# Performance work log

Hardware: AMD Instinct MI355X
Metric: run time of the kernel (lower is better)

## Reference

```python
import jax, jax.numpy as jnp
import numpy as np

N_NODES = 50000
N_EDGES = 800000
IN_DIM = 256
OUT_DIM = 64
HEADS = 4
NEG_SLOPE = 0.2  # PyG GATConv default


def setup_inputs() -> dict:
    key = jax.random.key(0)
    k_x, k_e, k_w, k_as, k_ad = jax.random.split(key, 5)
    x = jax.random.normal(k_x, (N_NODES, IN_DIM), dtype=jnp.float32)
    edge_index = jax.random.randint(k_e, (2, N_EDGES), 0, N_NODES, dtype=jnp.int64)
    # Glorot-ish scaled params (as in PyG GATConv)
    W = jax.random.normal(k_w, (IN_DIM, HEADS * OUT_DIM), dtype=jnp.float32) / np.sqrt(IN_DIM)
    att_src = jax.random.normal(k_as, (HEADS, OUT_DIM), dtype=jnp.float32) / np.sqrt(OUT_DIM)
    att_dst = jax.random.normal(k_ad, (HEADS, OUT_DIM), dtype=jnp.float32) / np.sqrt(OUT_DIM)
    bias = jnp.zeros((HEADS * OUT_DIM,), dtype=jnp.float32)
    return {"x": x, "edge_index": edge_index, "W": W,
            "att_src": att_src, "att_dst": att_dst, "bias": bias}


def reference(x, edge_index, W, att_src, att_dst, bias):
    N = x.shape[0]
    H, C = att_src.shape
    # add self-loops (PyG GATConv default add_self_loops=True)
    loop = jnp.arange(N, dtype=edge_index.dtype)
    src = jnp.concatenate([edge_index[0], loop])  # [E+N] message sources j
    dst = jnp.concatenate([edge_index[1], loop])  # [E+N] message targets i

    xh = (x @ W).reshape(N, H, C)                 # [N, H, C]
    a_src = jnp.einsum('nhc,hc->nh', xh, att_src)  # [N, H]
    a_dst = jnp.einsum('nhc,hc->nh', xh, att_dst)  # [N, H]

    logits = jax.nn.leaky_relu(a_src[src] + a_dst[dst], NEG_SLOPE)  # [E+N, H]
    # segment softmax over incoming edges of each destination node
    seg_max = jax.ops.segment_max(logits, dst, num_segments=N)      # [N, H]
    e = jnp.exp(logits - seg_max[dst])
    seg_sum = jax.ops.segment_sum(e, dst, num_segments=N)           # [N, H]
    alpha = e / seg_sum[dst]                                        # [E+N, H]

    # weighted scatter-aggregate of source features
    msgs = alpha[:, :, None] * xh[src]                              # [E+N, H, C]
    out = jax.ops.segment_sum(msgs, dst, num_segments=N)            # [N, H, C]
    out = out.reshape(N, H * C) + bias                              # concat heads + bias
    # h.dim() == 2 here, so the original's mean(dim=1) branch is not taken
    return out
```

## Files before the change

kernel.cpp:

```cpp
#include <hip/hip_runtime.h>

#define NEG_SLOPE 0.2f
#define LRELU(x) ((x) > 0.0f ? (x) : NEG_SLOPE * (x))

typedef short short8 __attribute__((ext_vector_type(8)));
typedef unsigned short ushort8 __attribute__((ext_vector_type(8)));
typedef float f32x4v __attribute__((ext_vector_type(4)));

__device__ __forceinline__ unsigned short f2bf(float f) {
  unsigned int u = __float_as_uint(f);
  unsigned int r = (u + 0x7FFFu + ((u >> 16) & 1u)) >> 16;
  return (unsigned short)r;
}

__device__ __forceinline__ float bf2f(unsigned short u) {
  return __uint_as_float(((unsigned int)u) << 16);
}

__device__ __forceinline__ unsigned int cvt_pk_bf16(float lo, float hi) {
  unsigned int r;
  asm("v_cvt_pk_bf16_f32 %0, %1, %2" : "=v"(r) : "v"(lo), "v"(hi));
  return r;
}

__device__ __forceinline__ void gload_lds16(const void* g, void* l) {
  __builtin_amdgcn_global_load_lds(
      (const __attribute__((address_space(1))) unsigned int*)g,
      (__attribute__((address_space(3))) unsigned int*)l, 16, 0, 0);
}

#define CBC 448
#define CBW 64
#define CBF 1024

__global__ __launch_bounds__(256) void fused_pre(
    const float* __restrict__ W, unsigned short* __restrict__ Wtb,
    const int* __restrict__ ei, int* __restrict__ deg,
    int* __restrict__ rank, int E) {
  int b = blockIdx.x;
  int tid = threadIdx.x;
  if (b < CBC) {
    for (int e = b * 256 + tid; e < E; e += CBC * 256)
      rank[e] = atomicAdd(&deg[ei[E + e]], 1);
  } else {
    int bb = b - CBC;
    for (int idx = bb * 256 + tid; idx < 256 * 256; idx += CBW * 256) {
      int n = idx >> 8, k = idx & 255;
      Wtb[n * 256 + k] = f2bf(W[k * 256 + n]);
    }
  }
}

__global__ __launch_bounds__(1024) void scan1_kernel(const int* __restrict__ deg,
                                                     int* __restrict__ row_start,
                                                     int* __restrict__ bsum, int N) {
  __shared__ int buf[1024];
  int i = blockIdx.x * 1024 + (int)threadIdx.x;
  int v = (i < N) ? deg[i] : 0;
  buf[threadIdx.x] = v;
  __syncthreads();
  int run = v;
  for (int off = 1; off < 1024; off <<= 1) {
    int t = ((int)threadIdx.x >= off) ? buf[threadIdx.x - off] : 0;
    __syncthreads();
    run += t;
    buf[threadIdx.x] = run;
    __syncthreads();
  }
  if (i < N) row_start[i] = run - v;
  if (threadIdx.x == 1023) bsum[blockIdx.x] = run;
}

__global__ __launch_bounds__(1024) void scan_off(int* __restrict__ row_start,
                                                 const int* __restrict__ bsum,
                                                 int nb, int N) {
  __shared__ int s_off;
  int b = blockIdx.x;
  if (threadIdx.x < 64) {
    int acc = 0;
    for (int j = (int)threadIdx.x; j < b; j += 64) acc += bsum[j];
    for (int off = 32; off; off >>= 1) acc += __shfl_down(acc, off, 64);
    if (threadIdx.x == 0) s_off = acc;
  }
  __syncthreads();
  int off = s_off;
  int i = b * 1024 + (int)threadIdx.x;
  if (i < N) row_start[i] += off;
  if (b == nb - 1 && threadIdx.x == 0) row_start[N] = off + bsum[b];
}

__global__ __launch_bounds__(256) void fill_kernel(
    const int* __restrict__ ei, const int* __restrict__ row_start,
    const int* __restrict__ rank, int* __restrict__ csr_src, int E) {
  for (int e = blockIdx.x * 256 + threadIdx.x; e < E; e += CBF * 256)
    csr_src[row_start[ei[E + e]] + rank[e]] = ei[e];
}

__global__ __launch_bounds__(256) void gemm_mfma(
    const float* __restrict__ Xf, const unsigned short* __restrict__ Wtb,
    const float* __restrict__ attS, const float* __restrict__ attD,
    unsigned short* __restrict__ XHb, float* __restrict__ a_src,
    float* __restrict__ a_dst, int N) {
  __shared__ unsigned short lA[128 * 32];
  __shared__ unsigned short lB[128 * 32];
  const int gb = blockIdx.x;
  const int tid = threadIdx.x;
  const int lane = tid & 63;
  const int wave = tid >> 6;
  const int m0 = ((gb >> 4) * 8 + (gb & 7)) * 128;
  const int n0 = ((gb >> 3) & 1) * 128;
  const int wr = (wave >> 1) * 64;
  const int wc = (wave & 1) * 64;

  f32x4v acc[4][4];
#pragma unroll
  for (int i = 0; i < 4; ++i)
#pragma unroll
    for (int j = 0; j < 4; ++j) acc[i][j] = (f32x4v)(0.0f);

  const int srow = tid >> 2;
  const int skb = (tid & 3) * 16;
  const float* ap0 = Xf + (size_t)min(m0 + (tid >> 2), N - 1) * 256 + (tid & 3) * 8;
  const float* ap1 = Xf + (size_t)min(m0 + 64 + (tid >> 2), N - 1) * 256 + (tid & 3) * 8;

  const char* WtC = (const char*)Wtb;
  char* lAc = (char*)&lA[0];
  char* lBc = (char*)&lB[0];
  const int ldsB0 = wave * 1024;
  const int lr = lane & 15;
  const int hq = lane >> 4;
  const int kq = hq * 16;

  float4 c0 = *reinterpret_cast<const float4*>(ap0);
  float4 c1 = *reinterpret_cast<const float4*>(ap0 + 4);
  float4 c2 = *reinterpret_cast<const float4*>(ap1);
  float4 c3 = *reinterpret_cast<const float4*>(ap1 + 4);

#pragma unroll
  for (int kk = 0; kk < 8; ++kk) {
    const int k0 = kk * 32;
    gload_lds16(WtC + (size_t)(n0 + srow) * 512 + (size_t)k0 * 2 + skb, lBc + ldsB0);
    gload_lds16(WtC + (size_t)(n0 + srow + 64) * 512 + (size_t)k0 * 2 + skb,
                lBc + ldsB0 + 4096);
    {
      uint4 w0, w1;
      w0.x = cvt_pk_bf16(c0.x, c0.y); w0.y = cvt_pk_bf16(c0.z, c0.w);
      w0.z = cvt_pk_bf16(c1.x, c1.y); w0.w = cvt_pk_bf16(c1.z, c1.w);
      w1.x = cvt_pk_bf16(c2.x, c2.y); w1.y = cvt_pk_bf16(c2.z, c2.w);
      w1.z = cvt_pk_bf16(c3.x, c3.y); w1.w = cvt_pk_bf16(c3.z, c3.w);
      *reinterpret_cast<uint4*>(lAc + tid * 16) = w0;
      *reinterpret_cast<uint4*>(lAc + 4096 + tid * 16) = w1;
    }
    if (kk < 7) {
      c0 = *reinterpret_cast<const float4*>(ap0 + k0 + 32);
      c1 = *reinterpret_cast<const float4*>(ap0 + k0 + 36);
      c2 = *reinterpret_cast<const float4*>(ap1 + k0 + 32);
      c3 = *reinterpret_cast<const float4*>(ap1 + k0 + 36);
    }
    __syncthreads();

    short8 a[4], b[4];
#pragma unroll
    for (int i = 0; i < 4; ++i)
      a[i] = *reinterpret_cast<const short8*>(lAc + (wr + i * 16 + lr) * 64 + kq);
#pragma unroll
    for (int j = 0; j < 4; ++j)
      b[j] = *reinterpret_cast<const short8*>(lBc + (wc + j * 16 + lr) * 64 + kq);
#pragma unroll
    for (int i = 0; i < 4; ++i)
#pragma unroll
      for (int j = 0; j < 4; ++j)
        acc[i][j] = __builtin_amdgcn_mfma_f32_16x16x32_bf16(a[i], b[j], acc[i][j], 0, 0, 0);
    __syncthreads();
  }

  const int h = (n0 + wc) >> 6;
  float ws_[4], wd_[4];
#pragma unroll
  for (int j = 0; j < 4; ++j) {
    ws_[j] = attS[h * 64 + j * 16 + lr];
    wd_[j] = attD[h * 64 + j * 16 + lr];
  }
  const int rbase = m0 + wr + hq * 4;

#pragma unroll
  for (int i = 0; i < 4; ++i) {
#pragma unroll
    for (int r = 0; r < 4; ++r) {
      float ps = 0.f, pd = 0.f;
#pragma unroll
      for (int j = 0; j < 4; ++j) {
        ps += acc[i][j][r] * ws_[j];
        pd += acc[i][j][r] * wd_[j];
      }
#pragma unroll
      for (int off = 1; off < 16; off <<= 1) {
        ps += __shfl_xor(ps, off, 64);
        pd += __shfl_xor(pd, off, 64);
      }
      int row = rbase + i * 16 + r;
      if (lr == 0 && row < N) {
        a_src[row * 4 + h] = ps;
        a_dst[row * 4 + h] = pd;
      }
    }
  }

#pragma unroll
  for (int i = 0; i < 4; ++i)
#pragma unroll
    for (int j = 0; j < 4; ++j) {
      int col = n0 + wc + j * 16 + lr;
#pragma unroll
      for (int r = 0; r < 4; ++r)
        XHb[(size_t)(rbase + i * 16 + r) * 256 + col] = f2bf(acc[i][j][r]);
    }
}

__global__ __launch_bounds__(256) void gat_agg(
    const unsigned short* __restrict__ XHb, const float* __restrict__ a_src,
    const float* __restrict__ a_dst, const int* __restrict__ row_start,
    const int* __restrict__ csr_src, const float* __restrict__ bias,
    float* __restrict__ out, int N) {
  int wid = threadIdx.x >> 6;
  int lane = threadIdx.x & 63;
  int node = blockIdx.x * 4 + wid;
  if (node >= N) return;

  const int half = lane >> 5;
  const int l5 = lane & 31;
  const int h = l5 >> 3;
  const int c = l5 << 3;
  const unsigned short* __restrict__ xrow = XHb + c;

  float ad_h = a_dst[node * 4 + h];
  float as_h = a_src[node * 4 + h];

  int start = row_start[node];
  int end = row_start[node + 1];

  float acc[8];
  float sw = 0.f;
  if (half == 0) {
    float wself = __expf(LRELU(as_h + ad_h));
    ushort8 sv = *reinterpret_cast<const ushort8*>(xrow + (size_t)node * 256);
#pragma unroll
    for (int k = 0; k < 8; ++k) acc[k] = wself * bf2f(sv[k]);
    sw = wself;
  } else {
#pragma unroll
    for (int k = 0; k < 8; ++k) acc[k] = 0.f;
  }

  int p = start;
  for (; p + 8 <= end; p += 8) {
    int s0 = csr_src[p + half];
    int s1 = csr_src[p + 2 + half];
    int s2 = csr_src[p + 4 + half];
    int s3 = csr_src[p + 6 + half];
    float a0 = a_src[s0 * 4 + h] + ad_h;
    float a1 = a_src[s1 * 4 + h] + ad_h;
    float a2 = a_src[s2 * 4 + h] + ad_h;
    float a3 = a_src[s3 * 4 + h] + ad_h;
    ushort8 u0 = *reinterpret_cast<const ushort8*>(xrow + (size_t)s0 * 256);
    ushort8 u1 = *reinterpret_cast<const ushort8*>(xrow + (size_t)s1 * 256);
    ushort8 u2 = *reinterpret_cast<const ushort8*>(xrow + (size_t)s2 * 256);
    ushort8 u3 = *reinterpret_cast<const ushort8*>(xrow + (size_t)s3 * 256);
    float w0 = __expf(LRELU(a0));
    float w1 = __expf(LRELU(a1));
    float w2 = __expf(LRELU(a2));
    float w3 = __expf(LRELU(a3));
#pragma unroll
    for (int k = 0; k < 8; ++k) {
      acc[k] += w0 * bf2f(u0[k]);
      acc[k] += w1 * bf2f(u1[k]);
      acc[k] += w2 * bf2f(u2[k]);
      acc[k] += w3 * bf2f(u3[k]);
    }
    sw += (w0 + w1) + (w2 + w3);
  }
#pragma unroll
  for (int k = 0; k < 4; ++k) {
    int idx = p + 2 * k + half;
    if (idx < end) {
      int s = csr_src[idx];
      float aa = a_src[s * 4 + h] + ad_h;
      ushort8 u = *reinterpret_cast<const ushort8*>(xrow + (size_t)s * 256);
      float ww = __expf(LRELU(aa));
#pragma unroll
      for (int q = 0; q < 8; ++q) acc[q] += ww * bf2f(u[q]);
      sw += ww;
    }
  }

  sw += __shfl_xor(sw, 32, 64);
#pragma unroll
  for (int k = 0; k < 8; ++k) acc[k] += __shfl_xor(acc[k], 32, 64);

  if (half == 0) {
    float inv = 1.0f / sw;
    float4 b0 = *reinterpret_cast<const float4*>(bias + c);
    float4 b1 = *reinterpret_cast<const float4*>(bias + c + 4);
    float4 o0, o1;
    o0.x = acc[0] * inv + b0.x; o0.y = acc[1] * inv + b0.y;
    o0.z = acc[2] * inv + b0.z; o0.w = acc[3] * inv + b0.w;
    o1.x = acc[4] * inv + b1.x; o1.y = acc[5] * inv + b1.y;
    o1.z = acc[6] * inv + b1.z; o1.w = acc[7] * inv + b1.w;
    *reinterpret_cast<float4*>(out + (size_t)node * 256 + c) = o0;
    *reinterpret_cast<float4*>(out + (size_t)node * 256 + c + 4) = o1;
  }
}

extern "C" void kernel_launch(void* const* d_in, const int* in_sizes, int n_in,
                              void* d_out, int out_size, void* d_ws, size_t ws_size,
                              hipStream_t stream) {
  const float* x    = (const float*)d_in[0];
  const int*   ei   = (const int*)d_in[1];
  const float* Wm   = (const float*)d_in[2];
  const float* attS = (const float*)d_in[3];
  const float* attD = (const float*)d_in[4];
  const float* bias = (const float*)d_in[5];
  float* out = (float*)d_out;

  const int N = in_sizes[0] / 256;
  const int E = in_sizes[1] / 2;
  const int Mp = (N + 1023) / 1024 * 1024;
  const int nb = (N + 1023) / 1024;

  char* w = (char*)d_ws;
  unsigned short* XHb = (unsigned short*)w;  w += (size_t)Mp * 256 * 2;
  unsigned short* Wtb = (unsigned short*)w;  w += (size_t)256 * 256 * 2;
  float* a_src = (float*)w;                  w += (size_t)N * 4 * 4;
  float* a_dst = (float*)w;                  w += (size_t)N * 4 * 4;
  int* deg = (int*)w;                        w += (size_t)N * 4;
  int* rank = (int*)w;                       w += (size_t)E * 4;
  int* row_start = (int*)w;                  w += ((size_t)(N + 1) * 4 + 255) / 256 * 256;
  int* bsum = (int*)w;                       w += ((size_t)nb * 4 + 255) / 256 * 256;
  int* csr_src = (int*)w;                    w += (size_t)E * 4;

  hipMemsetAsync(deg, 0, (size_t)N * 4, stream);

  fused_pre<<<CBC + CBW, 256, 0, stream>>>(Wm, Wtb, ei, deg, rank, E);

  scan1_kernel<<<nb, 1024, 0, stream>>>(deg, row_start, bsum, N);
  scan_off<<<nb, 1024, 0, stream>>>(row_start, bsum, nb, N);

  const int nGemm = 2 * (Mp / 128);
  gemm_mfma<<<nGemm, 256, 0, stream>>>(x, Wtb, attS, attD, XHb, a_src, a_dst, N);

  fill_kernel<<<CBF, 256, 0, stream>>>(ei, row_start, rank, csr_src, E);

  gat_agg<<<(N + 3) / 4, 256, 0, stream>>>(XHb, a_src, a_dst, row_start, csr_src,
                                           bias, out, N);
}
```

Baseline: 156.0 us.

## Fuse degree counting into GEMM launch and use atomic-offset single-pass scan

Replaces the memset with a prep kernel that zeroes degrees while transposing W. Degree-counting blocks are merged into the GEMM launch so the atomics overlap with MFMA work. The two-kernel scan becomes one kernel in which each block claims its offset with an atomicAdd on a global total, giving per-block contiguous but non-sorted CSR segments. Aggregation reads end as start+deg. The aim is fewer kernel launches and less serialization, at the cost of a larger combined grid and a node order in the CSR that no longer follows block index.

```diff
diff --git a/kernel.cpp b/kernel.cpp
--- a/kernel.cpp
+++ b/kernel.cpp
@@ -30,81 +30,39 @@
 }
 
 #define CBC 448
-#define CBW 64
 #define CBF 1024
 
-__global__ __launch_bounds__(256) void fused_pre(
+__global__ __launch_bounds__(256) void prep_kernel(
     const float* __restrict__ W, unsigned short* __restrict__ Wtb,
-    const int* __restrict__ ei, int* __restrict__ deg,
-    int* __restrict__ rank, int E) {
-  int b = blockIdx.x;
-  int tid = threadIdx.x;
-  if (b < CBC) {
-    for (int e = b * 256 + tid; e < E; e += CBC * 256)
-      rank[e] = atomicAdd(&deg[ei[E + e]], 1);
-  } else {
-    int bb = b - CBC;
-    for (int idx = bb * 256 + tid; idx < 256 * 256; idx += CBW * 256) {
-      int n = idx >> 8, k = idx & 255;
-      Wtb[n * 256 + k] = f2bf(W[k * 256 + n]);
-    }
-  }
-}
-
-__global__ __launch_bounds__(1024) void scan1_kernel(const int* __restrict__ deg,
-                                                     int* __restrict__ row_start,
-                                                     int* __restrict__ bsum, int N) {
-  __shared__ int buf[1024];
-  int i = blockIdx.x * 1024 + (int)threadIdx.x;
-  int v = (i < N) ? deg[i] : 0;
-  buf[threadIdx.x] = v;
-  __syncthreads();
-  int run = v;
-  for (int off = 1; off < 1024; off <<= 1) {
-    int t = ((int)threadIdx.x >= off) ? buf[threadIdx.x - off] : 0;
-    __syncthreads();
-    run += t;
-    buf[threadIdx.x] = run;
-    __syncthreads();
-  }
-  if (i < N) row_start[i] = run - v;
-  if (threadIdx.x == 1023) bsum[blockIdx.x] = run;
-}
-
-__global__ __launch_bounds__(1024) void scan_off(int* __restrict__ row_start,
-                                                 const int* __restrict__ bsum,
-                                                 int nb, int N) {
-  __shared__ int s_off;
-  int b = blockIdx.x;
-  if (threadIdx.x < 64) {
-    int acc = 0;
-    for (int j = (int)threadIdx.x; j < b; j += 64) acc += bsum[j];
-    for (int off = 32; off; off >>= 1) acc += __shfl_down(acc, off, 64);
-    if (threadIdx.x == 0) s_off = acc;
-  }
-  __syncthreads();
-  int off = s_off;
-  int i = b * 1024 + (int)threadIdx.x;
-  if (i < N) row_start[i] += off;
-  if (b == nb - 1 && threadIdx.x == 0) row_start[N] = off + bsum[b];
-}
-
-__global__ __launch_bounds__(256) void fill_kernel(
-    const int* __restrict__ ei, const int* __restrict__ row_start,
-    const int* __restrict__ rank, int* __restrict__ csr_src, int E) {
-  for (int e = blockIdx.x * 256 + threadIdx.x; e < E; e += CBF * 256)
-    csr_src[row_start[ei[E + e]] + rank[e]] = ei[e];
-}
-
-__global__ __launch_bounds__(256) void gemm_mfma(
+    int* __restrict__ deg, int* __restrict__ gtotal, int N) {
+  int t = blockIdx.x * 256 + threadIdx.x;
+  for (int idx = t; idx < 256 * 256; idx += 64 * 256) {
+    int n = idx >> 8, k = idx & 255;
+    Wtb[n * 256 + k] = f2bf(W[k * 256 + n]);
+  }
+  for (int i = t; i < N; i += 64 * 256) deg[i] = 0;
+  if (t == 0) *gtotal = 0;
+}
+
+__global__ __launch_bounds__(256) void fused_cg(
     const float* __restrict__ Xf, const unsigned short* __restrict__ Wtb,
     const float* __restrict__ attS, const float* __restrict__ attD,
     unsigned short* __restrict__ XHb, float* __restrict__ a_src,
-    float* __restrict__ a_dst, int N) {
+    float* __restrict__ a_dst,
+    const int* __restrict__ ei, int* __restrict__ deg,
+    int* __restrict__ rank, int E, int N) {
   __shared__ unsigned short lA[128 * 32];
   __shared__ unsigned short lB[128 * 32];
-  const int gb = blockIdx.x;
+  const int bid = blockIdx.x;
   const int tid = threadIdx.x;
+
+  if (bid < CBC) {
+    for (int e = bid * 256 + tid; e < E; e += CBC * 256)
+      rank[e] = atomicAdd(&deg[ei[E + e]], 1);
+    return;
+  }
+
+  const int gb = bid - CBC;
   const int lane = tid & 63;
   const int wave = tid >> 6;
   const int m0 = ((gb >> 4) * 8 + (gb & 7)) * 128;
@@ -217,11 +175,40 @@
     }
 }
 
+__global__ __launch_bounds__(1024) void scan_alloc(const int* __restrict__ deg,
+                                                   int* __restrict__ row_start,
+                                                   int* __restrict__ gtotal, int N) {
+  __shared__ int buf[1024];
+  __shared__ int s_off;
+  int i = blockIdx.x * 1024 + (int)threadIdx.x;
+  int v = (i < N) ? deg[i] : 0;
+  buf[threadIdx.x] = v;
+  __syncthreads();
+  int run = v;
+  for (int off = 1; off < 1024; off <<= 1) {
+    int t = ((int)threadIdx.x >= off) ? buf[threadIdx.x - off] : 0;
+    __syncthreads();
+    run += t;
+    buf[threadIdx.x] = run;
+    __syncthreads();
+  }
+  if (threadIdx.x == 1023) s_off = atomicAdd(gtotal, run);
+  __syncthreads();
+  if (i < N) row_start[i] = s_off + run - v;
+}
+
+__global__ __launch_bounds__(256) void fill_kernel(
+    const int* __restrict__ ei, const int* __restrict__ row_start,
+    const int* __restrict__ rank, int* __restrict__ csr_src, int E) {
+  for (int e = blockIdx.x * 256 + threadIdx.x; e < E; e += CBF * 256)
+    csr_src[row_start[ei[E + e]] + rank[e]] = ei[e];
+}
+
 __global__ __launch_bounds__(256) void gat_agg(
     const unsigned short* __restrict__ XHb, const float* __restrict__ a_src,
     const float* __restrict__ a_dst, const int* __restrict__ row_start,
-    const int* __restrict__ csr_src, const float* __restrict__ bias,
-    float* __restrict__ out, int N) {
+    const int* __restrict__ deg, const int* __restrict__ csr_src,
+    const float* __restrict__ bias, float* __restrict__ out, int N) {
   int wid = threadIdx.x >> 6;
   int lane = threadIdx.x & 63;
   int node = blockIdx.x * 4 + wid;
@@ -237,7 +224,7 @@
   float as_h = a_src[node * 4 + h];
 
   int start = row_start[node];
-  int end = row_start[node + 1];
+  int end = start + deg[node];
 
   float acc[8];
   float sw = 0.f;
@@ -335,21 +322,19 @@
   int* deg = (int*)w;                        w += (size_t)N * 4;
   int* rank = (int*)w;                       w += (size_t)E * 4;
   int* row_start = (int*)w;                  w += ((size_t)(N + 1) * 4 + 255) / 256 * 256;
-  int* bsum = (int*)w;                       w += ((size_t)nb * 4 + 255) / 256 * 256;
+  int* gtotal = (int*)w;                     w += 256;
   int* csr_src = (int*)w;                    w += (size_t)E * 4;
 
-  hipMemsetAsync(deg, 0, (size_t)N * 4, stream);
-
-  fused_pre<<<CBC + CBW, 256, 0, stream>>>(Wm, Wtb, ei, deg, rank, E);
-
-  scan1_kernel<<<nb, 1024, 0, stream>>>(deg, row_start, bsum, N);
-  scan_off<<<nb, 1024, 0, stream>>>(row_start, bsum, nb, N);
+  prep_kernel<<<64, 256, 0, stream>>>(Wm, Wtb, deg, gtotal, N);
 
   const int nGemm = 2 * (Mp / 128);
-  gemm_mfma<<<nGemm, 256, 0, stream>>>(x, Wtb, attS, attD, XHb, a_src, a_dst, N);
+  fused_cg<<<CBC + nGemm, 256, 0, stream>>>(x, Wtb, attS, attD, XHb, a_src, a_dst,
+                                            ei, deg, rank, E, N);
+
+  scan_alloc<<<nb, 1024, 0, stream>>>(deg, row_start, gtotal, N);
 
   fill_kernel<<<CBF, 256, 0, stream>>>(ei, row_start, rank, csr_src, E);
 
-  gat_agg<<<(N + 3) / 4, 256, 0, stream>>>(XHb, a_src, a_dst, row_start, csr_src,
-                                           bias, out, N);
-}
+  gat_agg<<<(N + 3) / 4, 256, 0, stream>>>(XHb, a_src, a_dst, row_start, deg,
+                                           csr_src, bias, out, N);
+}
```

After: 149.5 us. -4.2%, faster.
